# Kernel tuning notes

Measured on AMD Instinct MI355X. Metric: run time of the kernel, lower is better.

## Reference

```python
import jax, jax.numpy as jnp
import numpy as np

SIZE = 7  # spatial size, matches init kwarg


def setup_inputs() -> dict:
    key = jax.random.key(0)
    k1, k2 = jax.random.split(key, 2)
    N, C, H, W = 256, 2048, SIZE, SIZE
    x = jax.random.normal(k1, (N, C, H, W), dtype=jnp.float32)
    # nn.Linear(2*C, 2): weight (2, 2C), bias (2,)
    Wlin = jax.random.normal(k2, (2, 2 * C), dtype=jnp.float32) * 0.02
    b = jnp.zeros((2,), dtype=jnp.float32)
    return {"x": x, "Wlin": Wlin, "b": b}


def reference(x, Wlin, b):
    N, C, H, W = x.shape
    HW = H * W
    size = SIZE
    # (N, HW, C) token view
    rx = x.reshape(N, C, HW).transpose(0, 2, 1)
    # index of max mean-activation token per sample
    idx = jnp.argmax(jnp.mean(rx, axis=-1), axis=-1)  # (N,)
    bidx = jnp.arange(N)
    max_feat = rx[bidx, idx]  # (N, C)
    # concat(max_feat, rx) @ Wlin.T + b, split to avoid materializing (N,HW,2C)
    W1, W2 = Wlin[:, :C], Wlin[:, C:]
    pred = jax.nn.relu(
        jnp.einsum('npc,oc->npo', rx, W2) + (max_feat @ W1.T)[:, None, :] + b
    )  # (N, HW, 2)
    # zero out prediction at the anchor token
    pred = pred.at[bidx, idx].set(0.0)
    # basic label grid (i, j)
    ii, jj = jnp.meshgrid(jnp.arange(H), jnp.arange(W), indexing='ij')
    label = jnp.stack([ii, jj], axis=-1).reshape(HW, 2).astype(x.dtype)  # (HW, 2)
    anchor = label[idx][:, None, :]  # (N, 1, 2)
    rel = (label[None, :, :] - anchor) / size  # (N, HW, 2)
    rel_dist = jnp.sqrt(jnp.sum(rel ** 2, axis=-1))  # (N, HW)
    rel_angle = (jnp.arctan2(rel[..., 1], rel[..., 0]) / jnp.pi + 1) / 2  # (N, HW)
    dist_loss = (pred[..., 0] - rel_dist) ** 2
    gap = pred[..., 1] - rel_angle
    gap = jnp.where(gap < 0, gap + 1, gap)
    gap = gap - jnp.mean(gap, axis=-1, keepdims=True)
    return (dist_loss + gap ** 2).reshape(N, H, W)
```

## Files before the change

### kernel.cpp

```cpp
#include <hip/hip_runtime.h>
#include <math.h>

#define N_BATCH 256
#define C_CH    2048
#define HW      49
#define SIZE7   7
#define BLOCK   1024
#define NWAVES  16
#define C_PER_W (C_CH / NWAVES)

__global__ __launch_bounds__(BLOCK) void rpp_fused_kernel(
    const float* __restrict__ x, const float* __restrict__ Wlin,
    const float* __restrict__ b, float* __restrict__ out) {
  const int n    = blockIdx.x;
  const int tid  = threadIdx.x;
  const int lane = tid & 63;
  const int wave = tid >> 6;

  __shared__ __align__(16) float w_s[4][C_CH];
  __shared__ float red[NWAVES][5][64];

  for (int i = tid; i < 4 * C_CH; i += BLOCK) {
    const int q = i >> 11;
    const int c = i & (C_CH - 1);
    const int off = (q & 1) * (2 * C_CH) + (q >> 1) * C_CH;
    w_s[q][c] = Wlin[off + c];
  }
  __syncthreads();

  const int lp = (lane < HW) ? lane : 0;
  const int cb = wave * C_PER_W;
  const float* xp = x + (size_t)n * C_CH * HW + (size_t)cb * HW + lp;

  float a0 = 0.f, a1 = 0.f, a2 = 0.f, a3 = 0.f, a4 = 0.f;
#pragma unroll 2
  for (int c = 0; c < C_PER_W; c += 8) {
    const float v0 = xp[0 * HW];
    const float v1 = xp[1 * HW];
    const float v2 = xp[2 * HW];
    const float v3 = xp[3 * HW];
    const float v4 = xp[4 * HW];
    const float v5 = xp[5 * HW];
    const float v6 = xp[6 * HW];
    const float v7 = xp[7 * HW];
    xp += 8 * HW;
    const float4 wa0 = *(const float4*)&w_s[0][cb + c];
    const float4 wa1 = *(const float4*)&w_s[0][cb + c + 4];
    const float4 wb0 = *(const float4*)&w_s[1][cb + c];
    const float4 wb1 = *(const float4*)&w_s[1][cb + c + 4];
    const float4 wc0 = *(const float4*)&w_s[2][cb + c];
    const float4 wc1 = *(const float4*)&w_s[2][cb + c + 4];
    const float4 wd0 = *(const float4*)&w_s[3][cb + c];
    const float4 wd1 = *(const float4*)&w_s[3][cb + c + 4];
    a0 += ((v0 + v1) + (v2 + v3)) + ((v4 + v5) + (v6 + v7));
    a1 = fmaf(v0, wa0.x, fmaf(v1, wa0.y, fmaf(v2, wa0.z, fmaf(v3, wa0.w, a1))));
    a1 = fmaf(v4, wa1.x, fmaf(v5, wa1.y, fmaf(v6, wa1.z, fmaf(v7, wa1.w, a1))));
    a2 = fmaf(v0, wb0.x, fmaf(v1, wb0.y, fmaf(v2, wb0.z, fmaf(v3, wb0.w, a2))));
    a2 = fmaf(v4, wb1.x, fmaf(v5, wb1.y, fmaf(v6, wb1.z, fmaf(v7, wb1.w, a2))));
    a3 = fmaf(v0, wc0.x, fmaf(v1, wc0.y, fmaf(v2, wc0.z, fmaf(v3, wc0.w, a3))));
    a3 = fmaf(v4, wc1.x, fmaf(v5, wc1.y, fmaf(v6, wc1.z, fmaf(v7, wc1.w, a3))));
    a4 = fmaf(v0, wd0.x, fmaf(v1, wd0.y, fmaf(v2, wd0.z, fmaf(v3, wd0.w, a4))));
    a4 = fmaf(v4, wd1.x, fmaf(v5, wd1.y, fmaf(v6, wd1.z, fmaf(v7, wd1.w, a4))));
  }

  red[wave][0][lane] = a0;
  red[wave][1][lane] = a1;
  red[wave][2][lane] = a2;
  red[wave][3][lane] = a3;
  red[wave][4][lane] = a4;
  __syncthreads();

  if (tid < 5 * 64) {
    const int q = tid >> 6;
    const int l = tid & 63;
    float s = 0.f;
#pragma unroll
    for (int w = 0; w < NWAVES; w++) s += red[w][q][l];
    red[0][q][l] = s;
  }
  __syncthreads();

  if (wave == 0) {
    const float s0 = red[0][0][lane];
    const float s1 = red[0][1][lane];
    const float s2 = red[0][2][lane];
    const float s3 = red[0][3][lane];
    const float s4 = red[0][4][lane];

    float v = (lane < HW) ? s0 : -INFINITY;
    int vi = lane;
#pragma unroll
    for (int off = 32; off; off >>= 1) {
      const float ov = __shfl_down(v, off);
      const int oi = __shfl_down(vi, off);
      if (ov > v || (ov == v && oi < vi)) { v = ov; vi = oi; }
    }
    const int idx = __shfl(vi, 0);

    const float anc0 = __shfl(s1, idx);
    const float anc1 = __shfl(s2, idx);
    const float b0 = b[0], b1 = b[1];

    float pred0 = fmaxf(s3 + anc0 + b0, 0.f);
    float pred1 = fmaxf(s4 + anc1 + b1, 0.f);
    if (lane == idx) { pred0 = 0.f; pred1 = 0.f; }

    const int li = lane / SIZE7, lj = lane % SIZE7;
    const int ai = idx / SIZE7, aj = idx % SIZE7;
    const float ri = (float)(li - ai) * (1.0f / SIZE7);
    const float rj = (float)(lj - aj) * (1.0f / SIZE7);
    const float rdist = sqrtf(ri * ri + rj * rj);
    const float rangle = atan2f(rj, ri) * 0.15915494309189535f + 0.5f;

    float dl = pred0 - rdist;
    dl *= dl;
    float gap = pred1 - rangle;
    if (gap < 0.f) gap += 1.f;

    float g = (lane < HW) ? gap : 0.f;
#pragma unroll
    for (int off = 32; off; off >>= 1) g += __shfl_down(g, off);
    const float mean = __shfl(g, 0) * (1.0f / HW);
    gap -= mean;

    if (lane < HW) out[(size_t)n * HW + lane] = dl + gap * gap;
  }
}

extern "C" void kernel_launch(void* const* d_in, const int* in_sizes, int n_in,
                              void* d_out, int out_size, void* d_ws, size_t ws_size,
                              hipStream_t stream) {
  const float* x    = (const float*)d_in[0];
  const float* Wlin = (const float*)d_in[1];
  const float* b    = (const float*)d_in[2];
  float* out = (float*)d_out;
  (void)d_ws; (void)ws_size;

  hipLaunchKernelGGL(rpp_fused_kernel, dim3(N_BATCH), dim3(BLOCK), 0,
                     stream, x, Wlin, b, out);
}
```

Measured before the change: 153.7 us.

## Double-buffer x tiles into LDS via async global_load_lds and read weights uniformly

Replaces direct per-lane strided global loads of x with contiguous 16-byte async global-to-LDS copies of channel tiles, double-buffered so the next tile loads while the current one is reduced. Weights are no longer staged into shared memory; they are read via wave-uniform addresses (readfirstlane) from global memory, which frees LDS for the x tiles. This is meant to improve coalescing and overlap memory with compute, at the cost of extra barriers per tile and a large LDS footprint that holds occupancy to one block per CU.

```diff
diff --git a/kernel.cpp b/kernel.cpp
--- a/kernel.cpp
+++ b/kernel.cpp
@@ -7,7 +7,11 @@
 #define SIZE7   7
 #define BLOCK   1024
 #define NWAVES  16
-#define C_PER_W (C_CH / NWAVES)
+#define TC      256
+#define NT      (C_CH / TC)
+#define TILE_F  (TC * HW)
+#define TILE_V4 (TILE_F / 4)
+#define CPWT    (TC / NWAVES)
 
 __global__ __launch_bounds__(BLOCK) void rpp_fused_kernel(
     const float* __restrict__ x, const float* __restrict__ Wlin,
@@ -17,50 +21,59 @@
   const int lane = tid & 63;
   const int wave = tid >> 6;
 
-  __shared__ __align__(16) float w_s[4][C_CH];
+  __shared__ __align__(16) float xs[2][TILE_F];
   __shared__ float red[NWAVES][5][64];
 
-  for (int i = tid; i < 4 * C_CH; i += BLOCK) {
-    const int q = i >> 11;
-    const int c = i & (C_CH - 1);
-    const int off = (q & 1) * (2 * C_CH) + (q >> 1) * C_CH;
-    w_s[q][c] = Wlin[off + c];
-  }
+  const size_t xbase = (size_t)n * (C_CH * HW);
+  const int lp = (lane < HW) ? lane : 0;
+
+#define STAGE(DB, T)                                                          \
+  do {                                                                        \
+    const float* gsrc_ = x + xbase + (size_t)(T) * TILE_F;                    \
+    for (int k_ = 0; k_ < 4; ++k_) {                                          \
+      const int i_ = tid + k_ * BLOCK;                                        \
+      if (i_ < TILE_V4) {                                                     \
+        __builtin_amdgcn_global_load_lds(                                     \
+            (const __attribute__((address_space(1))) void*)(gsrc_ + i_ * 4),  \
+            (__attribute__((address_space(3))) void*)(&xs[DB][i_ * 4]),       \
+            16, 0, 0);                                                        \
+      }                                                                       \
+    }                                                                         \
+  } while (0)
+
+  float a0 = 0.f, a1 = 0.f, a2 = 0.f, a3 = 0.f, a4 = 0.f;
+
+  STAGE(0, 0);
+  asm volatile("s_waitcnt vmcnt(0)" ::: "memory");
   __syncthreads();
 
-  const int lp = (lane < HW) ? lane : 0;
-  const int cb = wave * C_PER_W;
-  const float* xp = x + (size_t)n * C_CH * HW + (size_t)cb * HW + lp;
+  int db = 0;
+  for (int t = 0; t < NT; ++t) {
+    if (t + 1 < NT) STAGE(db ^ 1, t + 1);
 
-  float a0 = 0.f, a1 = 0.f, a2 = 0.f, a3 = 0.f, a4 = 0.f;
-#pragma unroll 2
-  for (int c = 0; c < C_PER_W; c += 8) {
-    const float v0 = xp[0 * HW];
-    const float v1 = xp[1 * HW];
-    const float v2 = xp[2 * HW];
-    const float v3 = xp[3 * HW];
-    const float v4 = xp[4 * HW];
-    const float v5 = xp[5 * HW];
-    const float v6 = xp[6 * HW];
-    const float v7 = xp[7 * HW];
-    xp += 8 * HW;
-    const float4 wa0 = *(const float4*)&w_s[0][cb + c];
-    const float4 wa1 = *(const float4*)&w_s[0][cb + c + 4];
-    const float4 wb0 = *(const float4*)&w_s[1][cb + c];
-    const float4 wb1 = *(const float4*)&w_s[1][cb + c + 4];
-    const float4 wc0 = *(const float4*)&w_s[2][cb + c];
-    const float4 wc1 = *(const float4*)&w_s[2][cb + c + 4];
-    const float4 wd0 = *(const float4*)&w_s[3][cb + c];
-    const float4 wd1 = *(const float4*)&w_s[3][cb + c + 4];
-    a0 += ((v0 + v1) + (v2 + v3)) + ((v4 + v5) + (v6 + v7));
-    a1 = fmaf(v0, wa0.x, fmaf(v1, wa0.y, fmaf(v2, wa0.z, fmaf(v3, wa0.w, a1))));
-    a1 = fmaf(v4, wa1.x, fmaf(v5, wa1.y, fmaf(v6, wa1.z, fmaf(v7, wa1.w, a1))));
-    a2 = fmaf(v0, wb0.x, fmaf(v1, wb0.y, fmaf(v2, wb0.z, fmaf(v3, wb0.w, a2))));
-    a2 = fmaf(v4, wb1.x, fmaf(v5, wb1.y, fmaf(v6, wb1.z, fmaf(v7, wb1.w, a2))));
-    a3 = fmaf(v0, wc0.x, fmaf(v1, wc0.y, fmaf(v2, wc0.z, fmaf(v3, wc0.w, a3))));
-    a3 = fmaf(v4, wc1.x, fmaf(v5, wc1.y, fmaf(v6, wc1.z, fmaf(v7, wc1.w, a3))));
-    a4 = fmaf(v0, wd0.x, fmaf(v1, wd0.y, fmaf(v2, wd0.z, fmaf(v3, wd0.w, a4))));
-    a4 = fmaf(v4, wd1.x, fmaf(v5, wd1.y, fmaf(v6, wd1.z, fmaf(v7, wd1.w, a4))));
+    const float* xsl = &xs[db][wave * CPWT * HW + lp];
+    const int c0 = t * TC + wave * CPWT;
+#pragma unroll
+    for (int k = 0; k < CPWT; k += 4) {
+      const int cu = __builtin_amdgcn_readfirstlane(c0 + k);
+      const float4 wA = *(const float4*)(Wlin + cu);
+      const float4 wB = *(const float4*)(Wlin + 2 * C_CH + cu);
+      const float4 wC = *(const float4*)(Wlin + C_CH + cu);
+      const float4 wD = *(const float4*)(Wlin + 3 * C_CH + cu);
+      const float v0 = xsl[(k + 0) * HW];
+      const float v1 = xsl[(k + 1) * HW];
+      const float v2 = xsl[(k + 2) * HW];
+      const float v3 = xsl[(k + 3) * HW];
+      a0 += (v0 + v1) + (v2 + v3);
+      a1 = fmaf(v0, wA.x, fmaf(v1, wA.y, fmaf(v2, wA.z, fmaf(v3, wA.w, a1))));
+      a2 = fmaf(v0, wB.x, fmaf(v1, wB.y, fmaf(v2, wB.z, fmaf(v3, wB.w, a2))));
+      a3 = fmaf(v0, wC.x, fmaf(v1, wC.y, fmaf(v2, wC.z, fmaf(v3, wC.w, a3))));
+      a4 = fmaf(v0, wD.x, fmaf(v1, wD.y, fmaf(v2, wD.z, fmaf(v3, wD.w, a4))));
+    }
+
+    asm volatile("s_waitcnt vmcnt(0)" ::: "memory");
+    __syncthreads();
+    db ^= 1;
   }
 
   red[wave][0][lane] = a0;
@@ -125,6 +138,7 @@
 
     if (lane < HW) out[(size_t)n * HW + lane] = dl + gap * gap;
   }
+#undef STAGE
 }
 
 extern "C" void kernel_launch(void* const* d_in, const int* in_sizes, int n_in,
```

Measured after the change: 153.2 us. Within noise of the previous version (-0.3%).
